# Kernel optimization log

Measured on AMD Instinct MI355X. Metric: run time of the kernel, lower is better.

The kernel has to match this reference:

```python
import jax, jax.numpy as jnp
import numpy as np

N_HEAD = 12

def fillnan(x):
    return jnp.nan_to_num(x, nan=0.0, posinf=0.0, neginf=0.0)

def setup_inputs() -> dict:
    key = jax.random.key(0)
    k1, k2, k3 = jax.random.split(key, 3)
    B, T, C = 2, 2048, 768
    x = jax.random.normal(k1, (B, T, C), dtype=jnp.float32)
    W_attn = jax.random.normal(k2, (3 * C, C), dtype=jnp.float32) * 0.02
    W_proj = jax.random.normal(k3, (C, C), dtype=jnp.float32) * 0.02
    return {"x": x, "W_attn": W_attn, "W_proj": W_proj}

def reference(x, W_attn, W_proj):
    B, T, C = x.shape
    H = N_HEAD
    D = C // H
    # qkv projection (torch Linear: x @ W^T), then nan-sanitize
    qkv = fillnan(jnp.einsum('btc,fc->btf', x, W_attn))  # [B,T,3C]
    q, k, v = jnp.split(qkv, 3, axis=-1)
    # [B,T,C] -> [B,H,T,D]
    q = q.reshape(B, T, H, D).transpose(0, 2, 1, 3)
    k = k.reshape(B, T, H, D).transpose(0, 2, 1, 3)
    v = v.reshape(B, T, H, D).transpose(0, 2, 1, 3)
    scale = 1.0 / np.sqrt(D).astype(np.float32)
    att = jnp.einsum('bhqd,bhkd->bhqk', q, k) * scale  # [B,H,T,T]
    att = fillnan(att)
    causal = jnp.tril(jnp.ones((T, T), dtype=bool))
    att = jnp.where(causal[None, None], att, -jnp.inf)
    att = jax.nn.softmax(att, axis=-1)
    att = fillnan(att)
    y = jnp.einsum('bhqk,bhkd->bhqd', att, v)  # [B,H,T,D]
    y = fillnan(y)
    y = y.transpose(0, 2, 1, 3).reshape(B, T, C)
    y = fillnan(jnp.einsum('btc,fc->btf', y, W_proj))
    return y
```

## Files before the change

### kernel.cpp

```cpp
#include <hip/hip_runtime.h>

typedef __attribute__((ext_vector_type(8))) short bf16x8;
typedef __attribute__((ext_vector_type(4))) float f32x4;

__device__ __forceinline__ unsigned short f2b(float f) {
  union { float f; unsigned u; } v; v.f = f;
  return (unsigned short)((v.u + 0x7FFFu + ((v.u >> 16) & 1u)) >> 16);
}
__device__ __forceinline__ unsigned short f2b_fast(float f) {
  union { float f; unsigned u; } v; v.f = f;
  return (unsigned short)((v.u + 0x8000u) >> 16);
}

#define XN4   786432
#define WAN4  442368
#define WPN4  147456
__global__ void cvt_all(const float* __restrict__ x, const float* __restrict__ Wa,
                        const float* __restrict__ Wp,
                        unsigned short* __restrict__ xb, unsigned short* __restrict__ Wab,
                        unsigned short* __restrict__ Wpb) {
  int i = blockIdx.x * 256 + threadIdx.x;
  const float* src; unsigned short* dst; int off;
  if (i < XN4)            { src = x;  dst = xb;  off = i; }
  else if (i < XN4 + WAN4){ src = Wa; dst = Wab; off = i - XN4; }
  else                    { src = Wp; dst = Wpb; off = i - XN4 - WAN4; }
  float4 f = reinterpret_cast<const float4*>(src)[off];
  ushort4 o;
  o.x = f2b(f.x); o.y = f2b(f.y); o.z = f2b(f.z); o.w = f2b(f.w);
  reinterpret_cast<ushort4*>(dst)[off] = o;
}

#define BM 128
#define BN 128
#define BK 64

__global__ __launch_bounds__(256, 2)
void gemm_nt(const unsigned short* __restrict__ A,
             const unsigned short* __restrict__ Bm,
             int M, int N, int K, int mode,
             unsigned short* __restrict__ qb,
             unsigned short* __restrict__ kb_,
             unsigned short* __restrict__ vt,
             float* __restrict__ outf) {
  __shared__ unsigned short As[BM * BK];
  __shared__ unsigned short Bs[BN * BK];
  int tid = threadIdx.x;
  int wave = tid >> 6, lane = tid & 63;
  int quad = lane >> 4, l16 = lane & 15;
  int m0 = blockIdx.x * BM, n0 = blockIdx.y * BN;
  int wm = (wave & 1) * 64, wn = (wave >> 1) * 64;

  int srow = lane >> 3;
  int scol = ((lane & 7) ^ srow) << 3;

  f32x4 acc[4][4] = {};

  for (int k0 = 0; k0 < K; k0 += BK) {
    __syncthreads();
#pragma unroll
    for (int i = 0; i < 4; ++i) {
      int r = wave * 32 + i * 8;
      __builtin_amdgcn_global_load_lds(
          (const __attribute__((address_space(1))) unsigned int*)(A + (size_t)(m0 + r + srow) * K + k0 + scol),
          (__attribute__((address_space(3))) unsigned int*)(As + r * BK), 16, 0, 0);
      __builtin_amdgcn_global_load_lds(
          (const __attribute__((address_space(1))) unsigned int*)(Bm + (size_t)(n0 + r + srow) * K + k0 + scol),
          (__attribute__((address_space(3))) unsigned int*)(Bs + r * BK), 16, 0, 0);
    }
    __syncthreads();
#pragma unroll
    for (int kb = 0; kb < 2; ++kb) {
      int ch = (((kb << 2) | quad) ^ (l16 & 7)) << 3;
      bf16x8 af[4], bf[4];
#pragma unroll
      for (int i = 0; i < 4; ++i)
        af[i] = *reinterpret_cast<const bf16x8*>(As + (wm + i * 16 + l16) * BK + ch);
#pragma unroll
      for (int j = 0; j < 4; ++j)
        bf[j] = *reinterpret_cast<const bf16x8*>(Bs + (wn + j * 16 + l16) * BK + ch);
#pragma unroll
      for (int i = 0; i < 4; ++i)
#pragma unroll
        for (int j = 0; j < 4; ++j)
          acc[i][j] = __builtin_amdgcn_mfma_f32_16x16x32_bf16(af[i], bf[j], acc[i][j], 0, 0, 0);
    }
  }

  const float scale2 = 0.125f * 1.44269504089f;
#pragma unroll
  for (int i = 0; i < 4; ++i) {
    int mbase = m0 + wm + i * 16 + quad * 4;
#pragma unroll
    for (int j = 0; j < 4; ++j) {
      int f = n0 + wn + j * 16 + l16;
#pragma unroll
      for (int r = 0; r < 4; ++r) {
        float c = acc[i][j][r];
        int m = mbase + r;
        if (mode == 0) {
          int b = m >> 11, t = m & 2047;
          int which = f / 768;
          int f2 = f - which * 768;
          int h = f2 >> 6, d = f2 & 63;
          int bh = b * 12 + h;
          if (which == 0)      qb[((size_t)(bh * 2048 + t)) * 64 + d] = f2b(c * scale2);
          else if (which == 1) kb_[((size_t)(bh * 2048 + t)) * 64 + d] = f2b(c);
          else                 vt[((size_t)(bh * 64 + d)) * 2048 + t] = f2b(c);
        } else {
          outf[(size_t)m * N + f] = c;
        }
      }
    }
  }
}

#define PLDP 72

__global__ __launch_bounds__(256, 4)
void attn_part(const unsigned short* __restrict__ Qb,
               const unsigned short* __restrict__ Kb,
               const unsigned short* __restrict__ Vt,
               float* __restrict__ Oacc, float* __restrict__ Lacc) {
  __shared__ unsigned short Ks[64 * 64];
  __shared__ unsigned short Vs[64 * 64];
  __shared__ unsigned short P[4 * 32 * PLDP];
  const int T = 2048, D = 64;
  int wave = threadIdx.x >> 6, lane = threadIdx.x & 63;
  int quad = lane >> 4, l16 = lane & 15;

  int w = blockIdx.x;
  int bh = w / 72;
  int r = w - bh * 72;
  int b = 0;
#pragma unroll
  for (int i = 0; i < 16; ++i) {
    int nb = (i >> 1) + 1;
    if (r >= nb) { r -= nb; b = i + 1; } else break;
  }
  int c = r;
  int q0 = b * 128;
  int qrow = q0 + wave * 32;
  int kbeg = c * 256;
  int kend = kbeg + 256; if (kend > q0 + 128) kend = q0 + 128;

  const unsigned short* Qp = Qb + (size_t)bh * T * D;
  const unsigned short* Kp = Kb + (size_t)bh * T * D;
  const unsigned short* Vp = Vt + (size_t)bh * D * T;
  unsigned short* Pw = P + wave * 32 * PLDP;

  int srow = lane >> 3;
  int scol = ((lane & 7) ^ srow) << 3;

  bf16x8 aq[2][2];
#pragma unroll
  for (int qi = 0; qi < 2; ++qi)
#pragma unroll
    for (int cc = 0; cc < 2; ++cc)
      aq[qi][cc] = *reinterpret_cast<const bf16x8*>(
          Qp + (qrow + qi * 16 + l16) * D + cc * 32 + quad * 8);

  bf16x8 ones;
#pragma unroll
  for (int e = 0; e < 8; ++e) ones[e] = (short)0x3F80;

  f32x4 o[2][4] = {};
  f32x4 lacc[2] = {};

  for (int k0 = kbeg; k0 < kend; k0 += 64) {
    __syncthreads();
#pragma unroll
    for (int i = 0; i < 2; ++i) {
      int rr = wave * 16 + i * 8;
      __builtin_amdgcn_global_load_lds(
          (const __attribute__((address_space(1))) unsigned int*)(Kp + (size_t)(k0 + rr + srow) * D + scol),
          (__attribute__((address_space(3))) unsigned int*)(Ks + rr * 64), 16, 0, 0);
      __builtin_amdgcn_global_load_lds(
          (const __attribute__((address_space(1))) unsigned int*)(Vp + (size_t)(rr + srow) * T + k0 + scol),
          (__attribute__((address_space(3))) unsigned int*)(Vs + rr * 64), 16, 0, 0);
    }
    __syncthreads();

    if (k0 > qrow + 31) continue;

    f32x4 sacc[2][4] = {};
#pragma unroll
    for (int nt = 0; nt < 4; ++nt) {
      bf16x8 bk0 = *reinterpret_cast<const bf16x8*>(Ks + (nt * 16 + l16) * 64 + ((quad ^ (l16 & 7)) << 3));
      bf16x8 bk1 = *reinterpret_cast<const bf16x8*>(Ks + (nt * 16 + l16) * 64 + (((4 | quad) ^ (l16 & 7)) << 3));
#pragma unroll
      for (int qi = 0; qi < 2; ++qi) {
        sacc[qi][nt] = __builtin_amdgcn_mfma_f32_16x16x32_bf16(aq[qi][0], bk0, sacc[qi][nt], 0, 0, 0);
        sacc[qi][nt] = __builtin_amdgcn_mfma_f32_16x16x32_bf16(aq[qi][1], bk1, sacc[qi][nt], 0, 0, 0);
      }
    }

    if (k0 + 63 > qrow) {
#pragma unroll
      for (int qi = 0; qi < 2; ++qi)
#pragma unroll
        for (int nt = 0; nt < 4; ++nt) {
          int col = k0 + nt * 16 + l16;
#pragma unroll
          for (int rr = 0; rr < 4; ++rr) {
            int row = qrow + qi * 16 + quad * 4 + rr;
            sacc[qi][nt][rr] = (col <= row) ? sacc[qi][nt][rr] : -1e30f;
          }
        }
    }
#pragma unroll
    for (int qi = 0; qi < 2; ++qi)
#pragma unroll
      for (int nt = 0; nt < 4; ++nt)
#pragma unroll
        for (int rr = 0; rr < 4; ++rr)
          sacc[qi][nt][rr] = exp2f(sacc[qi][nt][rr]);

#pragma unroll
    for (int qi = 0; qi < 2; ++qi)
#pragma unroll
      for (int nt = 0; nt < 4; ++nt)
#pragma unroll
        for (int rr = 0; rr < 4; ++rr)
          Pw[(qi * 16 + quad * 4 + rr) * PLDP + nt * 16 + l16] = f2b_fast(sacc[qi][nt][rr]);
    __asm__ volatile("s_waitcnt lgkmcnt(0)" ::: "memory");

    bf16x8 vf[4][2];
#pragma unroll
    for (int dt = 0; dt < 4; ++dt) {
      vf[dt][0] = *reinterpret_cast<const bf16x8*>(Vs + (dt * 16 + l16) * 64 + ((quad ^ (l16 & 7)) << 3));
      vf[dt][1] = *reinterpret_cast<const bf16x8*>(Vs + (dt * 16 + l16) * 64 + (((4 | quad) ^ (l16 & 7)) << 3));
    }
#pragma unroll
    for (int qi = 0; qi < 2; ++qi) {
      bf16x8 ap0 = *reinterpret_cast<const bf16x8*>(Pw + (qi * 16 + l16) * PLDP + quad * 8);
      bf16x8 ap1 = *reinterpret_cast<const bf16x8*>(Pw + (qi * 16 + l16) * PLDP + 32 + quad * 8);
#pragma unroll
      for (int dt = 0; dt < 4; ++dt) {
        o[qi][dt] = __builtin_amdgcn_mfma_f32_16x16x32_bf16(ap0, vf[dt][0], o[qi][dt], 0, 0, 0);
        o[qi][dt] = __builtin_amdgcn_mfma_f32_16x16x32_bf16(ap1, vf[dt][1], o[qi][dt], 0, 0, 0);
      }
      lacc[qi] = __builtin_amdgcn_mfma_f32_16x16x32_bf16(ap0, ones, lacc[qi], 0, 0, 0);
      lacc[qi] = __builtin_amdgcn_mfma_f32_16x16x32_bf16(ap1, ones, lacc[qi], 0, 0, 0);
    }
  }

#pragma unroll
  for (int qi = 0; qi < 2; ++qi)
#pragma unroll
    for (int dt = 0; dt < 4; ++dt)
#pragma unroll
      for (int rr = 0; rr < 4; ++rr) {
        int row = qrow + qi * 16 + quad * 4 + rr;
        atomicAdd(&Oacc[((size_t)(bh * T + row)) * 64 + dt * 16 + l16], o[qi][dt][rr]);
      }
  if (l16 == 0) {
#pragma unroll
    for (int qi = 0; qi < 2; ++qi)
#pragma unroll
      for (int rr = 0; rr < 4; ++rr)
        atomicAdd(&Lacc[bh * T + qrow + qi * 16 + quad * 4 + rr], lacc[qi][rr]);
  }
}

__global__ __launch_bounds__(256)
void attn_norm(const float* __restrict__ Oacc, const float* __restrict__ Lacc,
               unsigned short* __restrict__ Yb) {
  int g = blockIdx.x * 256 + threadIdx.x;
  int d4 = g & 15;
  int t = (g >> 4) & 2047;
  int bh = g >> 15;
  int b = bh / 12, h = bh - b * 12;
  float4 ov = reinterpret_cast<const float4*>(Oacc)[g];
  float rl = 1.0f / Lacc[bh * 2048 + t];
  ushort4 y;
  y.x = f2b(ov.x * rl); y.y = f2b(ov.y * rl);
  y.z = f2b(ov.z * rl); y.w = f2b(ov.w * rl);
  *reinterpret_cast<ushort4*>(Yb + ((size_t)(b * 2048 + t)) * 768 + h * 64 + d4 * 4) = y;
}

extern "C" void kernel_launch(void* const* d_in, const int* in_sizes, int n_in,
                              void* d_out, int out_size, void* d_ws, size_t ws_size,
                              hipStream_t stream) {
  const float* x  = (const float*)d_in[0];
  const float* Wa = (const float*)d_in[1];
  const float* Wp = (const float*)d_in[2];
  float* out = (float*)d_out;

  unsigned short* ws = (unsigned short*)d_ws;
  unsigned short* xb  = ws;
  unsigned short* Wab = xb  + 3145728;
  unsigned short* Wpb = Wab + 1769472;
  unsigned short* Qb  = Wpb + 589824;
  unsigned short* Kb  = Qb  + 3145728;
  unsigned short* Vt  = Kb  + 3145728;
  unsigned short* Yb  = Vt  + 3145728;
  float*          Oacc = (float*)(Yb + 3145728);
  float*          Lacc = Oacc + 3145728;

  hipMemsetAsync(Oacc, 0, (3145728 + 49152) * sizeof(float), stream);

  cvt_all<<<(XN4 + WAN4 + WPN4) / 256, 256, 0, stream>>>(x, Wa, Wp, xb, Wab, Wpb);

  gemm_nt<<<dim3(4096 / BM, 2304 / BN), 256, 0, stream>>>(
      xb, Wab, 4096, 2304, 768, 0, Qb, Kb, Vt, nullptr);

  attn_part<<<1728, 256, 0, stream>>>(Qb, Kb, Vt, Oacc, Lacc);
  attn_norm<<<786432 / 256, 256, 0, stream>>>(Oacc, Lacc, Yb);

  gemm_nt<<<dim3(4096 / BM, 768 / BN), 256, 0, stream>>>(
      Yb, Wpb, 4096, 768, 768, 1, nullptr, nullptr, nullptr, out);
}
```

Before: 179.5 us.

## Fuse attention normalization into projection GEMM and retune attention chunking

The single generic GEMM is split into specialized QKV and projection kernels. For V tiles the QKV kernel swaps the MFMA operands so the transposed V store is contiguous along t. Attention key chunks grow from 256 to 512, which means fewer blocks and fewer atomic partial sums, and the P scratch buffer moves from padding to an XOR swizzle. The separate normalization kernel is removed: the projection GEMM reads the fp32 partial outputs, divides by the row sums and converts to bf16 while staging its A tile, which saves a full Y round trip but puts fp32 loads into the GEMM's main loop.

```diff
diff --git a/kernel.cpp b/kernel.cpp
--- a/kernel.cpp
+++ b/kernel.cpp
@@ -30,25 +30,23 @@
   reinterpret_cast<ushort4*>(dst)[off] = o;
 }
 
-#define BM 128
-#define BN 128
 #define BK 64
 
 __global__ __launch_bounds__(256, 2)
-void gemm_nt(const unsigned short* __restrict__ A,
-             const unsigned short* __restrict__ Bm,
-             int M, int N, int K, int mode,
-             unsigned short* __restrict__ qb,
-             unsigned short* __restrict__ kb_,
-             unsigned short* __restrict__ vt,
-             float* __restrict__ outf) {
-  __shared__ unsigned short As[BM * BK];
-  __shared__ unsigned short Bs[BN * BK];
+void gemm_qkv(const unsigned short* __restrict__ A,
+              const unsigned short* __restrict__ Bm,
+              unsigned short* __restrict__ qb,
+              unsigned short* __restrict__ kb_,
+              unsigned short* __restrict__ vt) {
+  __shared__ unsigned short As[128 * 64];
+  __shared__ unsigned short Bs[128 * 64];
+  const int K = 768;
   int tid = threadIdx.x;
   int wave = tid >> 6, lane = tid & 63;
   int quad = lane >> 4, l16 = lane & 15;
-  int m0 = blockIdx.x * BM, n0 = blockIdx.y * BN;
+  int m0 = blockIdx.x * 128, n0 = blockIdx.y * 128;
   int wm = (wave & 1) * 64, wn = (wave >> 1) * 64;
+  bool vswap = (n0 >= 1536);
 
   int srow = lane >> 3;
   int scol = ((lane & 7) ^ srow) << 3;
@@ -62,10 +60,10 @@
       int r = wave * 32 + i * 8;
       __builtin_amdgcn_global_load_lds(
           (const __attribute__((address_space(1))) unsigned int*)(A + (size_t)(m0 + r + srow) * K + k0 + scol),
-          (__attribute__((address_space(3))) unsigned int*)(As + r * BK), 16, 0, 0);
+          (__attribute__((address_space(3))) unsigned int*)(As + r * 64), 16, 0, 0);
       __builtin_amdgcn_global_load_lds(
           (const __attribute__((address_space(1))) unsigned int*)(Bm + (size_t)(n0 + r + srow) * K + k0 + scol),
-          (__attribute__((address_space(3))) unsigned int*)(Bs + r * BK), 16, 0, 0);
+          (__attribute__((address_space(3))) unsigned int*)(Bs + r * 64), 16, 0, 0);
     }
     __syncthreads();
 #pragma unroll
@@ -74,47 +72,68 @@
       bf16x8 af[4], bf[4];
 #pragma unroll
       for (int i = 0; i < 4; ++i)
-        af[i] = *reinterpret_cast<const bf16x8*>(As + (wm + i * 16 + l16) * BK + ch);
+        af[i] = *reinterpret_cast<const bf16x8*>(As + (wm + i * 16 + l16) * 64 + ch);
 #pragma unroll
       for (int j = 0; j < 4; ++j)
-        bf[j] = *reinterpret_cast<const bf16x8*>(Bs + (wn + j * 16 + l16) * BK + ch);
-#pragma unroll
-      for (int i = 0; i < 4; ++i)
-#pragma unroll
-        for (int j = 0; j < 4; ++j)
-          acc[i][j] = __builtin_amdgcn_mfma_f32_16x16x32_bf16(af[i], bf[j], acc[i][j], 0, 0, 0);
+        bf[j] = *reinterpret_cast<const bf16x8*>(Bs + (wn + j * 16 + l16) * 64 + ch);
+      if (!vswap) {
+#pragma unroll
+        for (int i = 0; i < 4; ++i)
+#pragma unroll
+          for (int j = 0; j < 4; ++j)
+            acc[i][j] = __builtin_amdgcn_mfma_f32_16x16x32_bf16(af[i], bf[j], acc[i][j], 0, 0, 0);
+      } else {
+#pragma unroll
+        for (int i = 0; i < 4; ++i)
+#pragma unroll
+          for (int j = 0; j < 4; ++j)
+            acc[i][j] = __builtin_amdgcn_mfma_f32_16x16x32_bf16(bf[j], af[i], acc[i][j], 0, 0, 0);
+      }
     }
   }
 
   const float scale2 = 0.125f * 1.44269504089f;
-#pragma unroll
-  for (int i = 0; i < 4; ++i) {
-    int mbase = m0 + wm + i * 16 + quad * 4;
+  if (!vswap) {
+#pragma unroll
+    for (int i = 0; i < 4; ++i) {
+      int mbase = m0 + wm + i * 16 + quad * 4;
+#pragma unroll
+      for (int j = 0; j < 4; ++j) {
+        int f = n0 + wn + j * 16 + l16;
+        int which = f / 768;
+        int f2 = f - which * 768;
+        int h = f2 >> 6, d = f2 & 63;
+#pragma unroll
+        for (int r = 0; r < 4; ++r) {
+          int m = mbase + r;
+          int b = m >> 11, t = m & 2047;
+          int bh = b * 12 + h;
+          if (which == 0) qb[((size_t)(bh * 2048 + t)) * 64 + d] = f2b(acc[i][j][r] * scale2);
+          else            kb_[((size_t)(bh * 2048 + t)) * 64 + d] = f2b(acc[i][j][r]);
+        }
+      }
+    }
+  } else {
 #pragma unroll
     for (int j = 0; j < 4; ++j) {
-      int f = n0 + wn + j * 16 + l16;
-#pragma unroll
-      for (int r = 0; r < 4; ++r) {
-        float c = acc[i][j][r];
-        int m = mbase + r;
-        if (mode == 0) {
-          int b = m >> 11, t = m & 2047;
-          int which = f / 768;
-          int f2 = f - which * 768;
+      int fbase = n0 + wn + j * 16 + quad * 4 - 1536;
+#pragma unroll
+      for (int i = 0; i < 4; ++i) {
+        int t_g = m0 + wm + i * 16 + l16;
+        int b = t_g >> 11, t = t_g & 2047;
+#pragma unroll
+        for (int r = 0; r < 4; ++r) {
+          int f2 = fbase + r;
           int h = f2 >> 6, d = f2 & 63;
           int bh = b * 12 + h;
-          if (which == 0)      qb[((size_t)(bh * 2048 + t)) * 64 + d] = f2b(c * scale2);
-          else if (which == 1) kb_[((size_t)(bh * 2048 + t)) * 64 + d] = f2b(c);
-          else                 vt[((size_t)(bh * 64 + d)) * 2048 + t] = f2b(c);
-        } else {
-          outf[(size_t)m * N + f] = c;
+          vt[((size_t)(bh * 64 + d)) * 2048 + t] = f2b(acc[i][j][r]);
         }
       }
     }
   }
 }
 
-#define PLDP 72
+#define CK 512
 
 __global__ __launch_bounds__(256, 4)
 void attn_part(const unsigned short* __restrict__ Qb,
@@ -123,30 +142,31 @@
                float* __restrict__ Oacc, float* __restrict__ Lacc) {
   __shared__ unsigned short Ks[64 * 64];
   __shared__ unsigned short Vs[64 * 64];
-  __shared__ unsigned short P[4 * 32 * PLDP];
+  __shared__ unsigned short P[4 * 32 * 64];
   const int T = 2048, D = 64;
   int wave = threadIdx.x >> 6, lane = threadIdx.x & 63;
   int quad = lane >> 4, l16 = lane & 15;
 
   int w = blockIdx.x;
-  int bh = w / 72;
-  int r = w - bh * 72;
-  int b = 0;
+  int bh = w / 40;
+  int r = w - bh * 40;
+  int b = 15;
 #pragma unroll
   for (int i = 0; i < 16; ++i) {
-    int nb = (i >> 1) + 1;
-    if (r >= nb) { r -= nb; b = i + 1; } else break;
+    int nb = (i >> 2) + 1;
+    if (r < nb) { b = i; break; }
+    r -= nb;
   }
   int c = r;
   int q0 = b * 128;
   int qrow = q0 + wave * 32;
-  int kbeg = c * 256;
-  int kend = kbeg + 256; if (kend > q0 + 128) kend = q0 + 128;
+  int kbeg = c * CK;
+  int kend = kbeg + CK; if (kend > q0 + 128) kend = q0 + 128;
 
   const unsigned short* Qp = Qb + (size_t)bh * T * D;
   const unsigned short* Kp = Kb + (size_t)bh * T * D;
   const unsigned short* Vp = Vt + (size_t)bh * D * T;
-  unsigned short* Pw = P + wave * 32 * PLDP;
+  unsigned short* Pw = P + wave * 32 * 64;
 
   int srow = lane >> 3;
   int scol = ((lane & 7) ^ srow) << 3;
@@ -165,6 +185,7 @@
 
   f32x4 o[2][4] = {};
   f32x4 lacc[2] = {};
+  int pswr = (l16 & 7) ^ (l16 >> 3);
 
   for (int k0 = kbeg; k0 < kend; k0 += 64) {
     __syncthreads();
@@ -218,10 +239,13 @@
 #pragma unroll
     for (int qi = 0; qi < 2; ++qi)
 #pragma unroll
-      for (int nt = 0; nt < 4; ++nt)
-#pragma unroll
-        for (int rr = 0; rr < 4; ++rr)
-          Pw[(qi * 16 + quad * 4 + rr) * PLDP + nt * 16 + l16] = f2b_fast(sacc[qi][nt][rr]);
+      for (int rr = 0; rr < 4; ++rr) {
+        int prow = qi * 16 + quad * 4 + rr;
+        int psw = (prow & 7) ^ ((prow >> 3) & 1);
+#pragma unroll
+        for (int nt = 0; nt < 4; ++nt)
+          Pw[prow * 64 + (((nt * 2 + (l16 >> 3)) ^ psw) << 3) + (l16 & 7)] = f2b_fast(sacc[qi][nt][rr]);
+      }
     __asm__ volatile("s_waitcnt lgkmcnt(0)" ::: "memory");
 
     bf16x8 vf[4][2];
@@ -232,8 +256,8 @@
     }
 #pragma unroll
     for (int qi = 0; qi < 2; ++qi) {
-      bf16x8 ap0 = *reinterpret_cast<const bf16x8*>(Pw + (qi * 16 + l16) * PLDP + quad * 8);
-      bf16x8 ap1 = *reinterpret_cast<const bf16x8*>(Pw + (qi * 16 + l16) * PLDP + 32 + quad * 8);
+      bf16x8 ap0 = *reinterpret_cast<const bf16x8*>(Pw + (qi * 16 + l16) * 64 + ((quad ^ pswr) << 3));
+      bf16x8 ap1 = *reinterpret_cast<const bf16x8*>(Pw + (qi * 16 + l16) * 64 + (((4 | quad) ^ pswr) << 3));
 #pragma unroll
       for (int dt = 0; dt < 4; ++dt) {
         o[qi][dt] = __builtin_amdgcn_mfma_f32_16x16x32_bf16(ap0, vf[dt][0], o[qi][dt], 0, 0, 0);
@@ -262,20 +286,87 @@
   }
 }
 
-__global__ __launch_bounds__(256)
-void attn_norm(const float* __restrict__ Oacc, const float* __restrict__ Lacc,
-               unsigned short* __restrict__ Yb) {
-  int g = blockIdx.x * 256 + threadIdx.x;
-  int d4 = g & 15;
-  int t = (g >> 4) & 2047;
-  int bh = g >> 15;
-  int b = bh / 12, h = bh - b * 12;
-  float4 ov = reinterpret_cast<const float4*>(Oacc)[g];
-  float rl = 1.0f / Lacc[bh * 2048 + t];
-  ushort4 y;
-  y.x = f2b(ov.x * rl); y.y = f2b(ov.y * rl);
-  y.z = f2b(ov.z * rl); y.w = f2b(ov.w * rl);
-  *reinterpret_cast<ushort4*>(Yb + ((size_t)(b * 2048 + t)) * 768 + h * 64 + d4 * 4) = y;
+__global__ __launch_bounds__(256, 2)
+void gemm_proj(const float* __restrict__ Oacc, const float* __restrict__ Lacc,
+               const unsigned short* __restrict__ Wpb, float* __restrict__ out) {
+  __shared__ unsigned short As[64 * 64];
+  __shared__ unsigned short Bs[128 * 64];
+  int tid = threadIdx.x;
+  int wave = tid >> 6, lane = tid & 63;
+  int quad = lane >> 4, l16 = lane & 15;
+  int m0 = blockIdx.x * 64, n0 = blockIdx.y * 128;
+  int wm = (wave & 1) * 32, wn = (wave >> 1) * 64;
+
+  int srow = lane >> 3;
+  int scol = ((lane & 7) ^ srow) << 3;
+
+  int arow = tid >> 2;
+  int acg = (tid & 3) * 2;
+  int t_g = m0 + arow;
+  int bb = t_g >> 11, tt = t_g & 2047;
+  int asw = arow & 7;
+
+  f32x4 acc[2][4] = {};
+
+  for (int k0 = 0; k0 < 768; k0 += BK) {
+    int h = k0 >> 6;
+    const float* arp = Oacc + ((size_t)((bb * 12 + h) * 2048 + tt)) * 64 + acg * 8;
+    float rl = 1.0f / Lacc[(bb * 12 + h) * 2048 + tt];
+    float4 a0 = reinterpret_cast<const float4*>(arp)[0];
+    float4 a1 = reinterpret_cast<const float4*>(arp)[1];
+    float4 a2 = reinterpret_cast<const float4*>(arp)[2];
+    float4 a3 = reinterpret_cast<const float4*>(arp)[3];
+
+    __syncthreads();
+#pragma unroll
+    for (int i = 0; i < 4; ++i) {
+      int r = wave * 32 + i * 8;
+      __builtin_amdgcn_global_load_lds(
+          (const __attribute__((address_space(1))) unsigned int*)(Wpb + (size_t)(n0 + r + srow) * 768 + k0 + scol),
+          (__attribute__((address_space(3))) unsigned int*)(Bs + r * 64), 16, 0, 0);
+    }
+    bf16x8 p0, p1;
+    p0[0] = (short)f2b(a0.x * rl); p0[1] = (short)f2b(a0.y * rl);
+    p0[2] = (short)f2b(a0.z * rl); p0[3] = (short)f2b(a0.w * rl);
+    p0[4] = (short)f2b(a1.x * rl); p0[5] = (short)f2b(a1.y * rl);
+    p0[6] = (short)f2b(a1.z * rl); p0[7] = (short)f2b(a1.w * rl);
+    p1[0] = (short)f2b(a2.x * rl); p1[1] = (short)f2b(a2.y * rl);
+    p1[2] = (short)f2b(a2.z * rl); p1[3] = (short)f2b(a2.w * rl);
+    p1[4] = (short)f2b(a3.x * rl); p1[5] = (short)f2b(a3.y * rl);
+    p1[6] = (short)f2b(a3.z * rl); p1[7] = (short)f2b(a3.w * rl);
+    *reinterpret_cast<bf16x8*>(As + arow * 64 + ((acg ^ asw) << 3)) = p0;
+    *reinterpret_cast<bf16x8*>(As + arow * 64 + (((acg + 1) ^ asw) << 3)) = p1;
+    __syncthreads();
+
+#pragma unroll
+    for (int kb = 0; kb < 2; ++kb) {
+      int ch = (((kb << 2) | quad) ^ (l16 & 7)) << 3;
+      bf16x8 af[2], bf[4];
+#pragma unroll
+      for (int i = 0; i < 2; ++i)
+        af[i] = *reinterpret_cast<const bf16x8*>(As + (wm + i * 16 + l16) * 64 + ch);
+#pragma unroll
+      for (int j = 0; j < 4; ++j)
+        bf[j] = *reinterpret_cast<const bf16x8*>(Bs + (wn + j * 16 + l16) * 64 + ch);
+#pragma unroll
+      for (int i = 0; i < 2; ++i)
+#pragma unroll
+        for (int j = 0; j < 4; ++j)
+          acc[i][j] = __builtin_amdgcn_mfma_f32_16x16x32_bf16(af[i], bf[j], acc[i][j], 0, 0, 0);
+    }
+  }
+
+#pragma unroll
+  for (int i = 0; i < 2; ++i) {
+    int mbase = m0 + wm + i * 16 + quad * 4;
+#pragma unroll
+    for (int j = 0; j < 4; ++j) {
+      int col = n0 + wn + j * 16 + l16;
+#pragma unroll
+      for (int r = 0; r < 4; ++r)
+        out[(size_t)(mbase + r) * 768 + col] = acc[i][j][r];
+    }
+  }
 }
 
 extern "C" void kernel_launch(void* const* d_in, const int* in_sizes, int n_in,
@@ -293,20 +384,16 @@
   unsigned short* Qb  = Wpb + 589824;
   unsigned short* Kb  = Qb  + 3145728;
   unsigned short* Vt  = Kb  + 3145728;
-  unsigned short* Yb  = Vt  + 3145728;
-  float*          Oacc = (float*)(Yb + 3145728);
+  float*          Oacc = (float*)(Vt + 3145728);
   float*          Lacc = Oacc + 3145728;
 
   hipMemsetAsync(Oacc, 0, (3145728 + 49152) * sizeof(float), stream);
 
   cvt_all<<<(XN4 + WAN4 + WPN4) / 256, 256, 0, stream>>>(x, Wa, Wp, xb, Wab, Wpb);
 
-  gemm_nt<<<dim3(4096 / BM, 2304 / BN), 256, 0, stream>>>(
-      xb, Wab, 4096, 2304, 768, 0, Qb, Kb, Vt, nullptr);
-
-  attn_part<<<1728, 256, 0, stream>>>(Qb, Kb, Vt, Oacc, Lacc);
-  attn_norm<<<786432 / 256, 256, 0, stream>>>(Oacc, Lacc, Yb);
-
-  gemm_nt<<<dim3(4096 / BM, 768 / BN), 256, 0, stream>>>(
-      Yb, Wpb, 4096, 768, 768, 1, nullptr, nullptr, nullptr, out);
-}
+  gemm_qkv<<<dim3(32, 18), 256, 0, stream>>>(xb, Wab, Qb, Kb, Vt);
+
+  attn_part<<<960, 256, 0, stream>>>(Qb, Kb, Vt, Oacc, Lacc);
+
+  gemm_proj<<<dim3(64, 6), 256, 0, stream>>>(Oacc, Lacc, Wpb, out);
+}
```

Result: slower. 185.2 us (+3.2%).
